# Kernel optimization log

Hardware: AMD Instinct MI355X
Metric: run time of the kernel (lower is better)

The kernel has to match this reference:

```python
import jax, jax.numpy as jnp
import numpy as np

N = 100000   # nodes
E = 1600000  # edges
IN = 128     # in_dim
C = 32       # hidden_dim
H = 2        # heads1
G = 64       # graphs in batch
NEG_SLOPE = 0.2


def setup_inputs() -> dict:
    key = jax.random.key(0)
    ks = jax.random.split(key, 20)
    f = lambda k, shape: jax.random.normal(k, shape, dtype=jnp.float32) * 0.05
    return {
        "x": jax.random.normal(ks[0], (N, IN), dtype=jnp.float32),
        "edge_index": jax.random.randint(ks[1], (2, E), 0, N, dtype=jnp.int32),
        "batch": jnp.sort(jax.random.randint(ks[2], (N,), 0, G, dtype=jnp.int32)),
        # GATv2 layer 1: lin_l / lin_r [IN, H*C], att [H, C], bias [H*C]
        "Wl1": f(ks[3], (IN, H * C)), "Wr1": f(ks[4], (IN, H * C)),
        "att1": f(ks[5], (H, C)), "b1": f(ks[6], (H * C,)),
        # GATv2 layer 2: heads=1
        "Wl2": f(ks[7], (H * C, C)), "Wr2": f(ks[8], (H * C, C)),
        "att2": f(ks[9], (1, C)), "b2": f(ks[10], (C,)),
        # GlobalAttention gate_nn: Linear(C,C) -> ReLU -> Linear(C,1)
        "g1w": f(ks[11], (C, C)), "g1b": f(ks[12], (C,)),
        "g2w": f(ks[13], (C, 1)), "g2b": f(ks[14], (1,)),
        # MLP head
        "lin1w": f(ks[15], (C, C)), "lin1b": f(ks[16], (C,)),
        "lin2w": f(ks[17], (C, 1)), "lin2b": f(ks[18], (1,)),
    }


def _gatv2(x, src, dst, Wl, Wr, att, bias, heads, ch):
    """PyG GATv2Conv (concat=True, share_weights=False, eval mode)."""
    n = x.shape[0]
    xl = (x @ Wl).reshape(n, heads, ch)  # source transform (also the message)
    xr = (x @ Wr).reshape(n, heads, ch)  # target transform
    e = jax.nn.leaky_relu(xl[src] + xr[dst], negative_slope=NEG_SLOPE)  # [E,H,C]
    score = jnp.einsum('ehc,hc->eh', e, att)  # [E,H]
    # scatter-softmax over incoming edges of each destination node
    m = jax.ops.segment_max(score, dst, num_segments=n)
    m = jnp.where(jnp.isfinite(m), m, 0.0)  # nodes w/o in-edges
    ex = jnp.exp(score - m[dst])
    denom = jax.ops.segment_sum(ex, dst, num_segments=n)
    alpha = ex / denom[dst]  # [E,H]
    out = jax.ops.segment_sum(alpha[:, :, None] * xl[src], dst, num_segments=n)
    return out.reshape(n, heads * ch) + bias


def reference(x, edge_index, batch, Wl1, Wr1, att1, b1, Wl2, Wr2, att2, b2,
              g1w, g1b, g2w, g2b, lin1w, lin1b, lin2w, lin2b):
    src, dst = edge_index[0], edge_index[1]
    h = jax.nn.relu(_gatv2(x, src, dst, Wl1, Wr1, att1, b1, H, C))   # [N, H*C]
    h = jax.nn.relu(_gatv2(h, src, dst, Wl2, Wr2, att2, b2, 1, C))   # [N, C]
    # GlobalAttention pooling: softmax(gate_nn(h)) over nodes of each graph
    gate = jax.nn.relu(h @ g1w + g1b) @ g2w + g2b                     # [N,1]
    gm = jax.ops.segment_max(gate, batch, num_segments=G)
    gm = jnp.where(jnp.isfinite(gm), gm, 0.0)
    ge = jnp.exp(gate - gm[batch])
    gd = jax.ops.segment_sum(ge, batch, num_segments=G)
    attw = ge / gd[batch]                                             # [N,1]
    pooled = jax.ops.segment_sum(attw * h, batch, num_segments=G)     # [G,C]
    z = jax.nn.relu(pooled @ lin1w + lin1b)
    return (z @ lin2w + lin2b).squeeze(-1)                            # [G]
```

## Files before the change

kernel.cpp:

```cpp
#include <hip/hip_runtime.h>
#include <hip/hip_fp16.h>
#include <cfloat>
#include <cstdint>
#include <cstddef>

#define N_NODES 100000
#define N_EDGES 1600000
#define G_GRAPHS 64
#define BKT_SHIFT 9
#define BKT_NODES (1 << BKT_SHIFT)
#define NBKT ((N_NODES + BKT_NODES - 1) >> BKT_SHIFT)
#define BKT_STRIDE 12288
#define SRC_BITS 17

typedef _Float16 hvec2 __attribute__((ext_vector_type(2)));
typedef _Float16 hvec4 __attribute__((ext_vector_type(4)));
typedef _Float16 hvec8 __attribute__((ext_vector_type(8)));
typedef float f32x4 __attribute__((ext_vector_type(4)));

#define LOG2E 1.4426950408889634f

static __device__ __forceinline__ float fdot2(hvec2 a, hvec2 b, float c) {
#if __has_builtin(__builtin_amdgcn_fdot2)
  return __builtin_amdgcn_fdot2(a, b, c, false);
#else
  return fmaf((float)a.y, (float)b.y, fmaf((float)a.x, (float)b.x, c));
#endif
}

static __device__ __forceinline__ hvec2 leaky2(hvec2 v) {
  return __builtin_elementwise_max(v, v * (_Float16)0.2f);
}

static __device__ __forceinline__ float fast_exp2(float x) {
#if __has_builtin(__builtin_amdgcn_exp2f)
  return __builtin_amdgcn_exp2f(x);
#else
  return exp2f(x);
#endif
}

template <int CTRL>
static __device__ __forceinline__ float dppadd(float v) {
  const int vi = __builtin_bit_cast(int, v);
  const int ti = __builtin_amdgcn_update_dpp(0, vi, CTRL, 0xF, 0xF, true);
  return v + __builtin_bit_cast(float, ti);
}
static __device__ __forceinline__ float dpp_sum8(float v) {
  v = dppadd<0xB1>(v);
  v = dppadd<0x4E>(v);
  v = dppadd<0x141>(v);
  return v;
}

__launch_bounds__(256) __global__
void prepw2_kernel(const float* __restrict__ Wl1, const float* __restrict__ Wr1,
                   const float* __restrict__ Wl2, const float* __restrict__ Wr2,
                   __half* __restrict__ Wh1, __half* __restrict__ Wh2) {
  const int idx = blockIdx.x * 256 + threadIdx.x;
  if (idx < 2 * 128 * 64) {
    const int j2 = idx / 128;
    const int k = idx - j2 * 128;
    const int j = (j2 < 64) ? j2 : j2 - 64;
    const float v = (j2 < 64) ? Wl1[k * 64 + j] : Wr1[k * 64 + j];
    Wh1[idx] = __float2half(v);
  } else if (idx < 2 * 128 * 64 + 2 * 64 * 32) {
    const int i2 = idx - 2 * 128 * 64;
    const int j2 = i2 / 64;
    const int k = i2 - j2 * 64;
    const int j = (j2 < 32) ? j2 : j2 - 32;
    const float v = (j2 < 32) ? Wl2[k * 32 + j] : Wr2[k * 32 + j];
    Wh2[i2] = __float2half(v);
  }
}

template <int K, int J, bool FUSE>
__launch_bounds__(256) __global__
void gemm_mfma(const float* __restrict__ A, const __half* __restrict__ Wh,
               const float* __restrict__ bias, __half* __restrict__ O0,
               float* __restrict__ O1, int n) {
  constexpr int BM = 64;
  constexpr int KP = K + 8;
  constexpr int J2 = 2 * J;
  __shared__ __align__(16) __half Alds[BM][KP];
  __shared__ __align__(16) __half Wlds[J2][KP];
  const int tid = threadIdx.x;
  const int n0 = blockIdx.x * BM;

  for (int c = tid; c < J2 * (K / 8); c += 256) {
    const int j = c / (K / 8);
    const int k8 = c - j * (K / 8);
    const uint4 w = reinterpret_cast<const uint4*>(Wh)[c];
    *reinterpret_cast<uint4*>(&Wlds[j][k8 * 8]) = w;
  }
  for (int c = tid; c < BM * (K / 4); c += 256) {
    const int r = c / (K / 4);
    const int k4 = c - r * (K / 4);
    const int row = n0 + r;
    float4 v = make_float4(0.f, 0.f, 0.f, 0.f);
    if (row < n) {
      v = reinterpret_cast<const float4*>(A)[(size_t)row * (K / 4) + k4];
      if constexpr (FUSE) {
        const float4 b = reinterpret_cast<const float4*>(bias)[k4];
        v.x = fmaxf(v.x + b.x, 0.f);
        v.y = fmaxf(v.y + b.y, 0.f);
        v.z = fmaxf(v.z + b.z, 0.f);
        v.w = fmaxf(v.w + b.w, 0.f);
      }
    }
    const hvec4 h = {(_Float16)v.x, (_Float16)v.y, (_Float16)v.z,
                     (_Float16)v.w};
    *reinterpret_cast<hvec4*>(&Alds[r][k4 * 4]) = h;
  }
  __syncthreads();

  const int wv = tid >> 6;
  const int l = tid & 63;
  const int lr = l & 15;
  const int lk = l >> 4;

  hvec8 afrag[K / 32];
#pragma unroll
  for (int kc = 0; kc < K / 32; ++kc)
    afrag[kc] = *reinterpret_cast<const hvec8*>(
        &Alds[wv * 16 + lr][kc * 32 + 8 * lk]);

#pragma unroll
  for (int jt = 0; jt < J2 / 16; ++jt) {
    f32x4 acc = {0.f, 0.f, 0.f, 0.f};
#pragma unroll
    for (int kc = 0; kc < K / 32; ++kc) {
      const hvec8 b = *reinterpret_cast<const hvec8*>(
          &Wlds[jt * 16 + lr][kc * 32 + 8 * lk]);
      acc = __builtin_amdgcn_mfma_f32_16x16x32_f16(afrag[kc], b, acc, 0, 0, 0);
    }
    const int colt = jt * 16 + lr;
    const int rowb = n0 + wv * 16 + 4 * lk;
#pragma unroll
    for (int r = 0; r < 4; ++r) {
      const int row = rowb + r;
      if (row < n) {
        if (jt < J / 16)
          O0[(size_t)row * J + colt] = __float2half(acc[r]);
        else
          O1[(size_t)row * J + (colt - J)] = acc[r];
      }
    }
  }
}

__launch_bounds__(1024) __global__
void partA_kernel(const int* __restrict__ ei, int* __restrict__ bcursor,
                  int* __restrict__ staging) {
  __shared__ int lh[NBKT];
  __shared__ int lbase[NBKT];
  const int tid = threadIdx.x;
  for (int i = tid; i < NBKT; i += 1024) lh[i] = 0;
  __syncthreads();
  const int e0 = blockIdx.x * 4096 + tid;
  int pk[4], b[4];
#pragma unroll
  for (int k = 0; k < 4; ++k) {
    const int e = e0 + k * 1024;
    const bool ok = e < N_EDGES;
    const int s = ok ? ei[e] : 0;
    const int d = ok ? ei[N_EDGES + e] : 0;
    pk[k] = s | ((d & (BKT_NODES - 1)) << SRC_BITS);
    b[k] = ok ? (d >> BKT_SHIFT) : -1;
    if (ok) atomicAdd(&lh[b[k]], 1);
  }
  __syncthreads();
  for (int i = tid; i < NBKT; i += 1024) {
    const int c = lh[i];
    lbase[i] = i * BKT_STRIDE + (c ? atomicAdd(&bcursor[i], c) : 0);
    lh[i] = 0;
  }
  __syncthreads();
#pragma unroll
  for (int k = 0; k < 4; ++k) {
    if (b[k] >= 0) {
      const int p = lbase[b[k]] + atomicAdd(&lh[b[k]], 1);
      staging[p] = pk[k];
    }
  }
}

__launch_bounds__(256) __global__
void partB_kernel(const int* __restrict__ staging,
                  const int* __restrict__ bcursor, int2* __restrict__ rowdeg,
                  int* __restrict__ csr_src) {
  __shared__ int ldeg[BKT_NODES];
  __shared__ int lsc[256];
  const int b = blockIdx.x;
  const int tid = threadIdx.x;
  const int node0 = b << BKT_SHIFT;
  const int start = b * BKT_STRIDE;
  const int cnt = bcursor[b];
  if (tid < 64) csr_src[start + cnt + tid] = 0;
  ldeg[2 * tid] = 0;
  ldeg[2 * tid + 1] = 0;
  __syncthreads();
  for (int i = tid; i < cnt; i += 256)
    atomicAdd(&ldeg[staging[start + i] >> SRC_BITS], 1);
  __syncthreads();
  const int d0 = ldeg[2 * tid];
  const int d1 = ldeg[2 * tid + 1];
  const int psum = d0 + d1;
  lsc[tid] = psum;
  __syncthreads();
  for (int d = 1; d < 256; d <<= 1) {
    const int t = (tid >= d) ? lsc[tid - d] : 0;
    __syncthreads();
    lsc[tid] += t;
    __syncthreads();
  }
  const int ex = lsc[tid] - psum + start;
  const int n0 = node0 + 2 * tid;
  if (n0 < N_NODES)
    *reinterpret_cast<int4*>(&rowdeg[n0]) = make_int4(ex, d0, ex + d0, d1);
  __syncthreads();
  ldeg[2 * tid] = ex;
  ldeg[2 * tid + 1] = ex + d0;
  __syncthreads();
  for (int i = tid; i < cnt; i += 256) {
    const int pk = staging[start + i];
    const int p = atomicAdd(&ldeg[pk >> SRC_BITS], 1);
    csr_src[p] = pk & ((1 << SRC_BITS) - 1);
  }
}

__launch_bounds__(256) __global__
void gat1_kernel(const __half* __restrict__ xlh, const float* __restrict__ xr,
                 const float* __restrict__ att, const int2* __restrict__ rowdeg,
                 const int* __restrict__ csr_src, float* __restrict__ agg) {
  const int n =
      __builtin_amdgcn_readfirstlane(blockIdx.x * 4 + (threadIdx.x >> 6));
  if (n >= N_NODES) return;
  const int lane = threadIdx.x & 63;
  const int g = lane >> 4;
  const int m = lane & 15;
  const int2 rd = rowdeg[n];
  const int r0 = __builtin_amdgcn_readfirstlane(rd.x);
  const int dg = __builtin_amdgcn_readfirstlane(rd.y);

  const float4 xrf =
      *reinterpret_cast<const float4*>(xr + ((size_t)n << 6) + 4 * m);
  const hvec2 xh01 = {(_Float16)xrf.x, (_Float16)xrf.y};
  const hvec2 xh23 = {(_Float16)xrf.z, (_Float16)xrf.w};
  const float4 atf = *reinterpret_cast<const float4*>(att + 4 * m);
  const hvec2 at01 = {(_Float16)(atf.x * LOG2E), (_Float16)(atf.y * LOG2E)};
  const hvec2 at23 = {(_Float16)(atf.z * LOG2E), (_Float16)(atf.w * LOG2E)};

  float s = 0.f, acc0 = 0.f, acc1 = 0.f, acc2 = 0.f, acc3 = 0.f;

  auto gather1 = [&](int sel) -> uint2 {
    return *reinterpret_cast<const uint2*>(
        (const char*)xlh + (((size_t)(unsigned)sel) << 7) + 8 * m);
  };
  auto compute1 = [&](int q, uint2 buf, int rem) {
    const hvec2 a01 = __builtin_bit_cast(hvec2, buf.x);
    const hvec2 a23 = __builtin_bit_cast(hvec2, buf.y);
    const hvec2 v01 = leaky2(a01 + xh01);
    const hvec2 v23 = leaky2(a23 + xh23);
    float p = fdot2(v23, at23, fdot2(v01, at01, 0.f));
    p = dpp_sum8(p);
    float e = fast_exp2(p);
    e = (4 * q + g < rem) ? e : 0.f;
    s += e;
    acc0 = fmaf(e, (float)a01.x, acc0);
    acc1 = fmaf(e, (float)a01.y, acc1);
    acc2 = fmaf(e, (float)a23.x, acc2);
    acc3 = fmaf(e, (float)a23.y, acc3);
  };

  for (int c0 = 0; c0 < dg; c0 += 64) {
    const int rem = dg - c0;
    const int* cp = csr_src + r0 + c0 + (lane >> 4);
    const int Kc = (min(rem, 64) + 3) >> 2;
#pragma unroll
    for (int g0 = 0; g0 < 16; g0 += 4) {
      if (g0 < Kc) {
        int sq[4];
#pragma unroll
        for (int k = 0; k < 4; ++k) sq[k] = cp[4 * (g0 + k)];
        uint2 B[4];
#pragma unroll
        for (int k = 0; k < 4; ++k)
          if (g0 + k < Kc) B[k] = gather1(sq[k]);
#pragma unroll
        for (int k = 0; k < 4; ++k)
          if (g0 + k < Kc) compute1(g0 + k, B[k], rem);
      }
    }
  }

  s += __shfl_xor(s, 16);
  s += __shfl_xor(s, 32);
  acc0 += __shfl_xor(acc0, 16);
  acc0 += __shfl_xor(acc0, 32);
  acc1 += __shfl_xor(acc1, 16);
  acc1 += __shfl_xor(acc1, 32);
  acc2 += __shfl_xor(acc2, 16);
  acc2 += __shfl_xor(acc2, 32);
  acc3 += __shfl_xor(acc3, 16);
  acc3 += __shfl_xor(acc3, 32);
  const float inv = s > 0.f ? 1.f / s : 0.f;
  if (g == 0)
    *reinterpret_cast<float4*>(agg + ((size_t)n << 6) + 4 * m) =
        make_float4(acc0 * inv, acc1 * inv, acc2 * inv, acc3 * inv);
}

__launch_bounds__(256) __global__
void gat2_kernel(const __half* __restrict__ xlh, const float* __restrict__ xr,
                 const float* __restrict__ att, const int2* __restrict__ rowdeg,
                 const int* __restrict__ csr_src, const float* __restrict__ b2,
                 float* __restrict__ h2) {
  const int n =
      __builtin_amdgcn_readfirstlane(blockIdx.x * 4 + (threadIdx.x >> 6));
  if (n >= N_NODES) return;
  const int lane = threadIdx.x & 63;
  const int g = lane >> 3;
  const int m = lane & 7;
  const int2 rd = rowdeg[n];
  const int r0 = __builtin_amdgcn_readfirstlane(rd.x);
  const int dg = __builtin_amdgcn_readfirstlane(rd.y);

  const float4 xrf =
      *reinterpret_cast<const float4*>(xr + (size_t)n * 32 + 4 * m);
  const hvec2 xh01 = {(_Float16)xrf.x, (_Float16)xrf.y};
  const hvec2 xh23 = {(_Float16)xrf.z, (_Float16)xrf.w};
  const float4 atf = *reinterpret_cast<const float4*>(att + 4 * m);
  const hvec2 at01 = {(_Float16)(atf.x * LOG2E), (_Float16)(atf.y * LOG2E)};
  const hvec2 at23 = {(_Float16)(atf.z * LOG2E), (_Float16)(atf.w * LOG2E)};

  float s = 0.f, acc0 = 0.f, acc1 = 0.f, acc2 = 0.f, acc3 = 0.f;

  auto gather1 = [&](int sel) -> uint2 {
    return *reinterpret_cast<const uint2*>(
        (const char*)xlh + (((size_t)(unsigned)sel) << 6) + 8 * m);
  };
  auto compute1 = [&](int q, uint2 buf, int rem) {
    const hvec2 a01 = __builtin_bit_cast(hvec2, buf.x);
    const hvec2 a23 = __builtin_bit_cast(hvec2, buf.y);
    const hvec2 v01 = leaky2(a01 + xh01);
    const hvec2 v23 = leaky2(a23 + xh23);
    float p = fdot2(v23, at23, fdot2(v01, at01, 0.f));
    p = dpp_sum8(p);
    float e = fast_exp2(p);
    e = (8 * q + g < rem) ? e : 0.f;
    s += e;
    acc0 = fmaf(e, (float)a01.x, acc0);
    acc1 = fmaf(e, (float)a01.y, acc1);
    acc2 = fmaf(e, (float)a23.x, acc2);
    acc3 = fmaf(e, (float)a23.y, acc3);
  };

  for (int c0 = 0; c0 < dg; c0 += 64) {
    const int rem = dg - c0;
    const int* cp = csr_src + r0 + c0 + (lane >> 3);
    const int Kc = (min(rem, 64) + 7) >> 3;
#pragma unroll
    for (int g0 = 0; g0 < 8; g0 += 4) {
      if (g0 < Kc) {
        int sq[4];
#pragma unroll
        for (int k = 0; k < 4; ++k) sq[k] = cp[8 * (g0 + k)];
        uint2 B[4];
#pragma unroll
        for (int k = 0; k < 4; ++k)
          if (g0 + k < Kc) B[k] = gather1(sq[k]);
#pragma unroll
        for (int k = 0; k < 4; ++k)
          if (g0 + k < Kc) compute1(g0 + k, B[k], rem);
      }
    }
  }

  s += __shfl_xor(s, 8);
  s += __shfl_xor(s, 16);
  s += __shfl_xor(s, 32);
  acc0 += __shfl_xor(acc0, 8);
  acc0 += __shfl_xor(acc0, 16);
  acc0 += __shfl_xor(acc0, 32);
  acc1 += __shfl_xor(acc1, 8);
  acc1 += __shfl_xor(acc1, 16);
  acc1 += __shfl_xor(acc1, 32);
  acc2 += __shfl_xor(acc2, 8);
  acc2 += __shfl_xor(acc2, 16);
  acc2 += __shfl_xor(acc2, 32);
  acc3 += __shfl_xor(acc3, 8);
  acc3 += __shfl_xor(acc3, 16);
  acc3 += __shfl_xor(acc3, 32);
  const float inv = s > 0.f ? 1.f / s : 0.f;
  const float4 b2v = *reinterpret_cast<const float4*>(b2 + 4 * m);
  if (g == 0)
    *reinterpret_cast<float4*>(h2 + (size_t)n * 32 + 4 * m) =
        make_float4(fmaxf(fmaf(acc0, inv, b2v.x), 0.f),
                    fmaxf(fmaf(acc1, inv, b2v.y), 0.f),
                    fmaxf(fmaf(acc2, inv, b2v.z), 0.f),
                    fmaxf(fmaf(acc3, inv, b2v.w), 0.f));
}

__launch_bounds__(256) __global__
void gate_kernel(const float* __restrict__ h2, const float* __restrict__ g1w,
                 const float* __restrict__ g1b, const float* __restrict__ g2w,
                 const float* __restrict__ g2b, float* __restrict__ gate) {
  __shared__ float Wg[32 * 32];
  __shared__ float Hs[8][32];
  const int tid = threadIdx.x;
  for (int i = tid; i < 1024; i += 256) Wg[i] = g1w[i];
  const int c = tid & 31;
  const int slot = tid >> 5;
  const int n = blockIdx.x * 8 + slot;
  Hs[slot][c] = (n < N_NODES) ? h2[(size_t)n * 32 + c] : 0.f;
  __syncthreads();
  float sg = g1b[c];
#pragma unroll
  for (int k4 = 0; k4 < 8; ++k4) {
    const float4 hq = *reinterpret_cast<const float4*>(&Hs[slot][4 * k4]);
    sg = fmaf(hq.x, Wg[(4 * k4 + 0) * 32 + c], sg);
    sg = fmaf(hq.y, Wg[(4 * k4 + 1) * 32 + c], sg);
    sg = fmaf(hq.z, Wg[(4 * k4 + 2) * 32 + c], sg);
    sg = fmaf(hq.w, Wg[(4 * k4 + 3) * 32 + c], sg);
  }
  sg = fmaxf(sg, 0.f);
  float pg = sg * g2w[c];
  pg += __shfl_xor(pg, 1);
  pg += __shfl_xor(pg, 2);
  pg += __shfl_xor(pg, 4);
  pg += __shfl_xor(pg, 8);
  pg += __shfl_xor(pg, 16);
  if (c == 0 && n < N_NODES) gate[n] = pg + g2b[0];
}

__launch_bounds__(256) __global__
void gepool_kernel(const float* __restrict__ h2, const int* __restrict__ batch,
                   const float* __restrict__ gate, float* __restrict__ gd,
                   float* __restrict__ pooled) {
  __shared__ float pool[G_GRAPHS * 32];
  __shared__ float gdb[G_GRAPHS];
  const int tid = threadIdx.x;
  for (int i = tid; i < G_GRAPHS * 32; i += 256) pool[i] = 0.f;
  if (tid < G_GRAPHS) gdb[tid] = 0.f;
  __syncthreads();
  const int c = tid & 31;
  const int hw = tid >> 5;
  const int start = blockIdx.x * 256;
  const int end = min(N_NODES, start + 256);
  for (int n = start + hw; n < end; n += 8) {
    const int b = batch[n];
    const float ge = __expf(gate[n]);
    atomicAdd(&pool[b * 32 + c], ge * h2[(size_t)n * 32 + c]);
    if (c == 0) atomicAdd(&gdb[b], ge);
  }
  __syncthreads();
  for (int i = tid; i < G_GRAPHS * 32; i += 256)
    if (pool[i] != 0.f) unsafeAtomicAdd(&pooled[i], pool[i]);
  if (tid < G_GRAPHS && gdb[tid] != 0.f) unsafeAtomicAdd(&gd[tid], gdb[tid]);
}

__launch_bounds__(64) __global__
void final_kernel(const float* __restrict__ pooled, const float* __restrict__ gd,
                  const float* __restrict__ l1w, const float* __restrict__ l1b,
                  const float* __restrict__ l2w, const float* __restrict__ l2b,
                  float* __restrict__ out) {
  const int g = blockIdx.x;
  const int lane = threadIdx.x;
  if (lane >= 32) return;
  const float invgd = 1.f / gd[g];
  float s = l1b[lane];
#pragma unroll
  for (int k = 0; k < 32; ++k)
    s = fmaf(pooled[g * 32 + k] * invgd, l1w[k * 32 + lane], s);
  s = fmaxf(s, 0.f);
  float p = s * l2w[lane];
  p += __shfl_xor(p, 1);
  p += __shfl_xor(p, 2);
  p += __shfl_xor(p, 4);
  p += __shfl_xor(p, 8);
  p += __shfl_xor(p, 16);
  if (lane == 0) out[g] = p + l2b[0];
}

extern "C" void kernel_launch(void* const* d_in, const int* in_sizes, int n_in,
                              void* d_out, int out_size, void* d_ws,
                              size_t ws_size, hipStream_t stream) {
  const float* x    = (const float*)d_in[0];
  const int*   ei   = (const int*)d_in[1];
  const int*   batch= (const int*)d_in[2];
  const float* Wl1  = (const float*)d_in[3];
  const float* Wr1  = (const float*)d_in[4];
  const float* att1 = (const float*)d_in[5];
  const float* b1   = (const float*)d_in[6];
  const float* Wl2  = (const float*)d_in[7];
  const float* Wr2  = (const float*)d_in[8];
  const float* att2 = (const float*)d_in[9];
  const float* b2   = (const float*)d_in[10];
  const float* g1w  = (const float*)d_in[11];
  const float* g1b  = (const float*)d_in[12];
  const float* g2w  = (const float*)d_in[13];
  const float* g2b  = (const float*)d_in[14];
  const float* l1w  = (const float*)d_in[15];
  const float* l1b  = (const float*)d_in[16];
  const float* l2w  = (const float*)d_in[17];
  const float* l2b  = (const float*)d_in[18];
  float* out = (float*)d_out;

  int* bcursor = (int*)d_ws;
  int2* rowdeg = (int2*)(bcursor + NBKT);
  int* csr_src = (int*)(rowdeg + N_NODES);
  int* staging = csr_src + (size_t)NBKT * BKT_STRIDE;
  float* fbase = (float*)(staging + (size_t)NBKT * BKT_STRIDE);
  float* xr1  = fbase;
  float* agg1 = xr1 + (size_t)N_NODES * 64;
  float* gate = agg1 + (size_t)N_NODES * 64;
  float* gd   = gate + N_NODES;
  float* pooled = gd + G_GRAPHS;
  __half* xl1h = (__half*)(pooled + G_GRAPHS * 32);
  __half* xl2h = xl1h;
  float* xr2 = xr1;
  float* h2  = xr1 + (size_t)N_NODES * 32;
  __half* Wh1 = (__half*)gate;
  __half* Wh2 = Wh1 + 128 * 128;

  (void)hipMemsetAsync(bcursor, 0, (size_t)NBKT * sizeof(int), stream);
  (void)hipMemsetAsync(gd, 0,
                       (size_t)(G_GRAPHS + G_GRAPHS * 32) * sizeof(float),
                       stream);

  prepw2_kernel<<<(2 * 128 * 64 + 2 * 64 * 32 + 255) / 256, 256, 0, stream>>>(
      Wl1, Wr1, Wl2, Wr2, Wh1, Wh2);

  partA_kernel<<<(N_EDGES + 4095) / 4096, 1024, 0, stream>>>(ei, bcursor,
                                                             staging);
  partB_kernel<<<NBKT, 256, 0, stream>>>(staging, bcursor, rowdeg, csr_src);

  gemm_mfma<128, 64, false><<<(N_NODES + 63) / 64, 256, 0, stream>>>(
      x, Wh1, nullptr, xl1h, xr1, N_NODES);
  gat1_kernel<<<(N_NODES + 3) / 4, 256, 0, stream>>>(xl1h, xr1, att1, rowdeg,
                                                     csr_src, agg1);

  gemm_mfma<64, 32, true><<<(N_NODES + 63) / 64, 256, 0, stream>>>(
      agg1, Wh2, b1, xl2h, xr2, N_NODES);
  gat2_kernel<<<(N_NODES + 3) / 4, 256, 0, stream>>>(xl2h, xr2, att2, rowdeg,
                                                     csr_src, b2, h2);
  gate_kernel<<<(N_NODES + 7) / 8, 256, 0, stream>>>(h2, g1w, g1b, g2w, g2b,
                                                     gate);

  gepool_kernel<<<(N_NODES + 255) / 256, 256, 0, stream>>>(h2, batch, gate, gd,
                                                           pooled);
  final_kernel<<<64, 64, 0, stream>>>(pooled, gd, l1w, l1b, l2w, l2b, out);
}
```

Measured before the change: 337.0 us.

## Merge small kernels to cut launches: fold weight prep, CSR build, gate and final

Folds the weight fp16 conversion into the edge-partition kernel and runs the CSR bucket build and the first GEMM as disjoint block ranges of one launch. The gate MLP is fused into the pooling kernel using wave shuffles, and the final MLP runs in the last block, picked by an atomic ticket. Two memsets become one. This removes about five launches and the gate round trip through global memory, at the cost of a last-block serial tail and more complex synchronisation.

```diff
diff --git a/kernel.cpp b/kernel.cpp
--- a/kernel.cpp
+++ b/kernel.cpp
@@ -53,108 +53,30 @@
   return v;
 }
 
-__launch_bounds__(256) __global__
-void prepw2_kernel(const float* __restrict__ Wl1, const float* __restrict__ Wr1,
-                   const float* __restrict__ Wl2, const float* __restrict__ Wr2,
-                   __half* __restrict__ Wh1, __half* __restrict__ Wh2) {
-  const int idx = blockIdx.x * 256 + threadIdx.x;
-  if (idx < 2 * 128 * 64) {
-    const int j2 = idx / 128;
-    const int k = idx - j2 * 128;
+__launch_bounds__(1024) __global__
+void partA_kernel(const int* __restrict__ ei, int* __restrict__ bcursor,
+                  int* __restrict__ staging,
+                  const float* __restrict__ Wl1, const float* __restrict__ Wr1,
+                  const float* __restrict__ Wl2, const float* __restrict__ Wr2,
+                  __half* __restrict__ Wh1, __half* __restrict__ Wh2) {
+  const int tid = threadIdx.x;
+  const int widx = blockIdx.x * 1024 + tid;
+  if (widx < 2 * 128 * 64) {
+    const int j2 = widx / 128;
+    const int k = widx - j2 * 128;
     const int j = (j2 < 64) ? j2 : j2 - 64;
-    const float v = (j2 < 64) ? Wl1[k * 64 + j] : Wr1[k * 64 + j];
-    Wh1[idx] = __float2half(v);
-  } else if (idx < 2 * 128 * 64 + 2 * 64 * 32) {
-    const int i2 = idx - 2 * 128 * 64;
+    Wh1[widx] =
+        __float2half((j2 < 64) ? Wl1[k * 64 + j] : Wr1[k * 64 + j]);
+  } else if (widx < 2 * 128 * 64 + 2 * 64 * 32) {
+    const int i2 = widx - 2 * 128 * 64;
     const int j2 = i2 / 64;
     const int k = i2 - j2 * 64;
     const int j = (j2 < 32) ? j2 : j2 - 32;
-    const float v = (j2 < 32) ? Wl2[k * 32 + j] : Wr2[k * 32 + j];
-    Wh2[i2] = __float2half(v);
-  }
-}
-
-template <int K, int J, bool FUSE>
-__launch_bounds__(256) __global__
-void gemm_mfma(const float* __restrict__ A, const __half* __restrict__ Wh,
-               const float* __restrict__ bias, __half* __restrict__ O0,
-               float* __restrict__ O1, int n) {
-  constexpr int BM = 64;
-  constexpr int KP = K + 8;
-  constexpr int J2 = 2 * J;
-  __shared__ __align__(16) __half Alds[BM][KP];
-  __shared__ __align__(16) __half Wlds[J2][KP];
-  const int tid = threadIdx.x;
-  const int n0 = blockIdx.x * BM;
-
-  for (int c = tid; c < J2 * (K / 8); c += 256) {
-    const int j = c / (K / 8);
-    const int k8 = c - j * (K / 8);
-    const uint4 w = reinterpret_cast<const uint4*>(Wh)[c];
-    *reinterpret_cast<uint4*>(&Wlds[j][k8 * 8]) = w;
-  }
-  for (int c = tid; c < BM * (K / 4); c += 256) {
-    const int r = c / (K / 4);
-    const int k4 = c - r * (K / 4);
-    const int row = n0 + r;
-    float4 v = make_float4(0.f, 0.f, 0.f, 0.f);
-    if (row < n) {
-      v = reinterpret_cast<const float4*>(A)[(size_t)row * (K / 4) + k4];
-      if constexpr (FUSE) {
-        const float4 b = reinterpret_cast<const float4*>(bias)[k4];
-        v.x = fmaxf(v.x + b.x, 0.f);
-        v.y = fmaxf(v.y + b.y, 0.f);
-        v.z = fmaxf(v.z + b.z, 0.f);
-        v.w = fmaxf(v.w + b.w, 0.f);
-      }
-    }
-    const hvec4 h = {(_Float16)v.x, (_Float16)v.y, (_Float16)v.z,
-                     (_Float16)v.w};
-    *reinterpret_cast<hvec4*>(&Alds[r][k4 * 4]) = h;
-  }
-  __syncthreads();
-
-  const int wv = tid >> 6;
-  const int l = tid & 63;
-  const int lr = l & 15;
-  const int lk = l >> 4;
-
-  hvec8 afrag[K / 32];
-#pragma unroll
-  for (int kc = 0; kc < K / 32; ++kc)
-    afrag[kc] = *reinterpret_cast<const hvec8*>(
-        &Alds[wv * 16 + lr][kc * 32 + 8 * lk]);
-
-#pragma unroll
-  for (int jt = 0; jt < J2 / 16; ++jt) {
-    f32x4 acc = {0.f, 0.f, 0.f, 0.f};
-#pragma unroll
-    for (int kc = 0; kc < K / 32; ++kc) {
-      const hvec8 b = *reinterpret_cast<const hvec8*>(
-          &Wlds[jt * 16 + lr][kc * 32 + 8 * lk]);
-      acc = __builtin_amdgcn_mfma_f32_16x16x32_f16(afrag[kc], b, acc, 0, 0, 0);
-    }
-    const int colt = jt * 16 + lr;
-    const int rowb = n0 + wv * 16 + 4 * lk;
-#pragma unroll
-    for (int r = 0; r < 4; ++r) {
-      const int row = rowb + r;
-      if (row < n) {
-        if (jt < J / 16)
-          O0[(size_t)row * J + colt] = __float2half(acc[r]);
-        else
-          O1[(size_t)row * J + (colt - J)] = acc[r];
-      }
-    }
-  }
-}
-
-__launch_bounds__(1024) __global__
-void partA_kernel(const int* __restrict__ ei, int* __restrict__ bcursor,
-                  int* __restrict__ staging) {
+    Wh2[i2] = __float2half((j2 < 32) ? Wl2[k * 32 + j] : Wr2[k * 32 + j]);
+  }
+
   __shared__ int lh[NBKT];
   __shared__ int lbase[NBKT];
-  const int tid = threadIdx.x;
   for (int i = tid; i < NBKT; i += 1024) lh[i] = 0;
   __syncthreads();
   const int e0 = blockIdx.x * 4096 + tid;
@@ -185,47 +107,193 @@
   }
 }
 
+#define GEMM1_K 128
+#define GEMM1_J 64
+#define SMEM_BYTES (64 * (GEMM1_K + 8) * 2 + 2 * GEMM1_J * (GEMM1_K + 8) * 2)
+
 __launch_bounds__(256) __global__
-void partB_kernel(const int* __restrict__ staging,
-                  const int* __restrict__ bcursor, int2* __restrict__ rowdeg,
-                  int* __restrict__ csr_src) {
-  __shared__ int ldeg[BKT_NODES];
-  __shared__ int lsc[256];
-  const int b = blockIdx.x;
+void partB_gemm1_kernel(const int* __restrict__ staging,
+                        const int* __restrict__ bcursor,
+                        int2* __restrict__ rowdeg, int* __restrict__ csr_src,
+                        const float* __restrict__ A,
+                        const __half* __restrict__ Wh,
+                        __half* __restrict__ O0, float* __restrict__ O1) {
+  __shared__ __align__(16) char smem[SMEM_BYTES];
   const int tid = threadIdx.x;
-  const int node0 = b << BKT_SHIFT;
-  const int start = b * BKT_STRIDE;
-  const int cnt = bcursor[b];
-  if (tid < 64) csr_src[start + cnt + tid] = 0;
-  ldeg[2 * tid] = 0;
-  ldeg[2 * tid + 1] = 0;
-  __syncthreads();
-  for (int i = tid; i < cnt; i += 256)
-    atomicAdd(&ldeg[staging[start + i] >> SRC_BITS], 1);
-  __syncthreads();
-  const int d0 = ldeg[2 * tid];
-  const int d1 = ldeg[2 * tid + 1];
-  const int psum = d0 + d1;
-  lsc[tid] = psum;
-  __syncthreads();
-  for (int d = 1; d < 256; d <<= 1) {
-    const int t = (tid >= d) ? lsc[tid - d] : 0;
+
+  if (blockIdx.x < NBKT) {
+    int* ldeg = (int*)smem;
+    int* lsc = (int*)(smem + BKT_NODES * 4);
+    const int b = blockIdx.x;
+    const int node0 = b << BKT_SHIFT;
+    const int start = b * BKT_STRIDE;
+    const int cnt = bcursor[b];
+    if (tid < 64) csr_src[start + cnt + tid] = 0;
+    ldeg[2 * tid] = 0;
+    ldeg[2 * tid + 1] = 0;
     __syncthreads();
-    lsc[tid] += t;
+    for (int i = tid; i < cnt; i += 256)
+      atomicAdd(&ldeg[staging[start + i] >> SRC_BITS], 1);
     __syncthreads();
-  }
-  const int ex = lsc[tid] - psum + start;
-  const int n0 = node0 + 2 * tid;
-  if (n0 < N_NODES)
-    *reinterpret_cast<int4*>(&rowdeg[n0]) = make_int4(ex, d0, ex + d0, d1);
-  __syncthreads();
-  ldeg[2 * tid] = ex;
-  ldeg[2 * tid + 1] = ex + d0;
-  __syncthreads();
-  for (int i = tid; i < cnt; i += 256) {
-    const int pk = staging[start + i];
-    const int p = atomicAdd(&ldeg[pk >> SRC_BITS], 1);
-    csr_src[p] = pk & ((1 << SRC_BITS) - 1);
+    const int d0 = ldeg[2 * tid];
+    const int d1 = ldeg[2 * tid + 1];
+    const int psum = d0 + d1;
+    lsc[tid] = psum;
+    __syncthreads();
+    for (int d = 1; d < 256; d <<= 1) {
+      const int t = (tid >= d) ? lsc[tid - d] : 0;
+      __syncthreads();
+      lsc[tid] += t;
+      __syncthreads();
+    }
+    const int ex = lsc[tid] - psum + start;
+    const int n0 = node0 + 2 * tid;
+    if (n0 < N_NODES)
+      *reinterpret_cast<int4*>(&rowdeg[n0]) = make_int4(ex, d0, ex + d0, d1);
+    __syncthreads();
+    ldeg[2 * tid] = ex;
+    ldeg[2 * tid + 1] = ex + d0;
+    __syncthreads();
+    for (int i = tid; i < cnt; i += 256) {
+      const int pk = staging[start + i];
+      const int p = atomicAdd(&ldeg[pk >> SRC_BITS], 1);
+      csr_src[p] = pk & ((1 << SRC_BITS) - 1);
+    }
+    return;
+  }
+
+  constexpr int K = GEMM1_K;
+  constexpr int J = GEMM1_J;
+  constexpr int KP = K + 8;
+  constexpr int J2 = 2 * J;
+  typedef __half(*AldsT)[KP];
+  AldsT Alds = (AldsT)smem;
+  AldsT Wlds = (AldsT)(smem + 64 * KP * 2);
+  const int n0 = (blockIdx.x - NBKT) * 64;
+
+  for (int c = tid; c < J2 * (K / 8); c += 256) {
+    const int j = c / (K / 8);
+    const int k8 = c - j * (K / 8);
+    const uint4 w = reinterpret_cast<const uint4*>(Wh)[c];
+    *reinterpret_cast<uint4*>(&Wlds[j][k8 * 8]) = w;
+  }
+  for (int c = tid; c < 64 * (K / 4); c += 256) {
+    const int r = c / (K / 4);
+    const int k4 = c - r * (K / 4);
+    const int row = n0 + r;
+    float4 v = make_float4(0.f, 0.f, 0.f, 0.f);
+    if (row < N_NODES)
+      v = reinterpret_cast<const float4*>(A)[(size_t)row * (K / 4) + k4];
+    const hvec4 h = {(_Float16)v.x, (_Float16)v.y, (_Float16)v.z,
+                     (_Float16)v.w};
+    *reinterpret_cast<hvec4*>(&Alds[r][k4 * 4]) = h;
+  }
+  __syncthreads();
+
+  const int wv = tid >> 6;
+  const int l = tid & 63;
+  const int lr = l & 15;
+  const int lk = l >> 4;
+
+  hvec8 afrag[K / 32];
+#pragma unroll
+  for (int kc = 0; kc < K / 32; ++kc)
+    afrag[kc] = *reinterpret_cast<const hvec8*>(
+        &Alds[wv * 16 + lr][kc * 32 + 8 * lk]);
+
+#pragma unroll
+  for (int jt = 0; jt < J2 / 16; ++jt) {
+    f32x4 acc = {0.f, 0.f, 0.f, 0.f};
+#pragma unroll
+    for (int kc = 0; kc < K / 32; ++kc) {
+      const hvec8 b = *reinterpret_cast<const hvec8*>(
+          &Wlds[jt * 16 + lr][kc * 32 + 8 * lk]);
+      acc = __builtin_amdgcn_mfma_f32_16x16x32_f16(afrag[kc], b, acc, 0, 0, 0);
+    }
+    const int colt = jt * 16 + lr;
+    const int rowb = n0 + wv * 16 + 4 * lk;
+#pragma unroll
+    for (int r = 0; r < 4; ++r) {
+      const int row = rowb + r;
+      if (row < N_NODES) {
+        if (jt < J / 16)
+          O0[(size_t)row * J + colt] = __float2half(acc[r]);
+        else
+          O1[(size_t)row * J + (colt - J)] = acc[r];
+      }
+    }
+  }
+}
+
+template <int K, int J>
+__launch_bounds__(256) __global__
+void gemm_mfma2(const float* __restrict__ A, const __half* __restrict__ Wh,
+                const float* __restrict__ bias, __half* __restrict__ O0,
+                float* __restrict__ O1) {
+  constexpr int KP = K + 8;
+  constexpr int J2 = 2 * J;
+  __shared__ __align__(16) __half Alds[64][KP];
+  __shared__ __align__(16) __half Wlds[J2][KP];
+  const int tid = threadIdx.x;
+  const int n0 = blockIdx.x * 64;
+
+  for (int c = tid; c < J2 * (K / 8); c += 256) {
+    const int j = c / (K / 8);
+    const int k8 = c - j * (K / 8);
+    const uint4 w = reinterpret_cast<const uint4*>(Wh)[c];
+    *reinterpret_cast<uint4*>(&Wlds[j][k8 * 8]) = w;
+  }
+  for (int c = tid; c < 64 * (K / 4); c += 256) {
+    const int r = c / (K / 4);
+    const int k4 = c - r * (K / 4);
+    const int row = n0 + r;
+    float4 v = make_float4(0.f, 0.f, 0.f, 0.f);
+    if (row < N_NODES) {
+      v = reinterpret_cast<const float4*>(A)[(size_t)row * (K / 4) + k4];
+      const float4 b = reinterpret_cast<const float4*>(bias)[k4];
+      v.x = fmaxf(v.x + b.x, 0.f);
+      v.y = fmaxf(v.y + b.y, 0.f);
+      v.z = fmaxf(v.z + b.z, 0.f);
+      v.w = fmaxf(v.w + b.w, 0.f);
+    }
+    const hvec4 h = {(_Float16)v.x, (_Float16)v.y, (_Float16)v.z,
+                     (_Float16)v.w};
+    *reinterpret_cast<hvec4*>(&Alds[r][k4 * 4]) = h;
+  }
+  __syncthreads();
+
+  const int wv = tid >> 6;
+  const int l = tid & 63;
+  const int lr = l & 15;
+  const int lk = l >> 4;
+
+  hvec8 afrag[K / 32];
+#pragma unroll
+  for (int kc = 0; kc < K / 32; ++kc)
+    afrag[kc] = *reinterpret_cast<const hvec8*>(
+        &Alds[wv * 16 + lr][kc * 32 + 8 * lk]);
+
+#pragma unroll
+  for (int jt = 0; jt < J2 / 16; ++jt) {
+    f32x4 acc = {0.f, 0.f, 0.f, 0.f};
+#pragma unroll
+    for (int kc = 0; kc < K / 32; ++kc) {
+      const hvec8 b = *reinterpret_cast<const hvec8*>(
+          &Wlds[jt * 16 + lr][kc * 32 + 8 * lk]);
+      acc = __builtin_amdgcn_mfma_f32_16x16x32_f16(afrag[kc], b, acc, 0, 0, 0);
+    }
+    const int colt = jt * 16 + lr;
+    const int rowb = n0 + wv * 16 + 4 * lk;
+#pragma unroll
+    for (int r = 0; r < 4; ++r) {
+      const int row = rowb + r;
+      if (row < N_NODES) {
+        if (jt < J / 16)
+          O0[(size_t)row * J + colt] = __float2half(acc[r]);
+        else
+          O1[(size_t)row * J + (colt - J)] = acc[r];
+      }
+    }
   }
 }
 
@@ -402,84 +470,88 @@
 }
 
 __launch_bounds__(256) __global__
-void gate_kernel(const float* __restrict__ h2, const float* __restrict__ g1w,
-                 const float* __restrict__ g1b, const float* __restrict__ g2w,
-                 const float* __restrict__ g2b, float* __restrict__ gate) {
+void gepool_final_kernel(const float* __restrict__ h2,
+                         const int* __restrict__ batch,
+                         const float* __restrict__ g1w,
+                         const float* __restrict__ g1b,
+                         const float* __restrict__ g2w,
+                         const float* __restrict__ g2b,
+                         float* __restrict__ gd, float* __restrict__ pooled,
+                         int* __restrict__ done,
+                         const float* __restrict__ l1w,
+                         const float* __restrict__ l1b,
+                         const float* __restrict__ l2w,
+                         const float* __restrict__ l2b,
+                         float* __restrict__ out) {
   __shared__ float Wg[32 * 32];
-  __shared__ float Hs[8][32];
+  __shared__ float pool[G_GRAPHS * 32];
+  __shared__ float gdb[G_GRAPHS];
+  __shared__ int lticket;
   const int tid = threadIdx.x;
   for (int i = tid; i < 1024; i += 256) Wg[i] = g1w[i];
-  const int c = tid & 31;
-  const int slot = tid >> 5;
-  const int n = blockIdx.x * 8 + slot;
-  Hs[slot][c] = (n < N_NODES) ? h2[(size_t)n * 32 + c] : 0.f;
-  __syncthreads();
-  float sg = g1b[c];
-#pragma unroll
-  for (int k4 = 0; k4 < 8; ++k4) {
-    const float4 hq = *reinterpret_cast<const float4*>(&Hs[slot][4 * k4]);
-    sg = fmaf(hq.x, Wg[(4 * k4 + 0) * 32 + c], sg);
-    sg = fmaf(hq.y, Wg[(4 * k4 + 1) * 32 + c], sg);
-    sg = fmaf(hq.z, Wg[(4 * k4 + 2) * 32 + c], sg);
-    sg = fmaf(hq.w, Wg[(4 * k4 + 3) * 32 + c], sg);
-  }
-  sg = fmaxf(sg, 0.f);
-  float pg = sg * g2w[c];
-  pg += __shfl_xor(pg, 1);
-  pg += __shfl_xor(pg, 2);
-  pg += __shfl_xor(pg, 4);
-  pg += __shfl_xor(pg, 8);
-  pg += __shfl_xor(pg, 16);
-  if (c == 0 && n < N_NODES) gate[n] = pg + g2b[0];
-}
-
-__launch_bounds__(256) __global__
-void gepool_kernel(const float* __restrict__ h2, const int* __restrict__ batch,
-                   const float* __restrict__ gate, float* __restrict__ gd,
-                   float* __restrict__ pooled) {
-  __shared__ float pool[G_GRAPHS * 32];
-  __shared__ float gdb[G_GRAPHS];
-  const int tid = threadIdx.x;
   for (int i = tid; i < G_GRAPHS * 32; i += 256) pool[i] = 0.f;
   if (tid < G_GRAPHS) gdb[tid] = 0.f;
   __syncthreads();
   const int c = tid & 31;
   const int hw = tid >> 5;
+  const float g1bc = g1b[c];
+  const float g2wc = g2w[c];
+  const float g2b0 = g2b[0];
   const int start = blockIdx.x * 256;
   const int end = min(N_NODES, start + 256);
   for (int n = start + hw; n < end; n += 8) {
     const int b = batch[n];
-    const float ge = __expf(gate[n]);
-    atomicAdd(&pool[b * 32 + c], ge * h2[(size_t)n * 32 + c]);
+    const float hval = h2[(size_t)n * 32 + c];
+    float sg = g1bc;
+#pragma unroll
+    for (int k = 0; k < 32; ++k)
+      sg = fmaf(__shfl(hval, k, 32), Wg[k * 32 + c], sg);
+    sg = fmaxf(sg, 0.f);
+    float pg = sg * g2wc;
+    pg += __shfl_xor(pg, 1);
+    pg += __shfl_xor(pg, 2);
+    pg += __shfl_xor(pg, 4);
+    pg += __shfl_xor(pg, 8);
+    pg += __shfl_xor(pg, 16);
+    const float ge = __expf(pg + g2b0);
+    atomicAdd(&pool[b * 32 + c], ge * hval);
     if (c == 0) atomicAdd(&gdb[b], ge);
   }
   __syncthreads();
   for (int i = tid; i < G_GRAPHS * 32; i += 256)
     if (pool[i] != 0.f) unsafeAtomicAdd(&pooled[i], pool[i]);
   if (tid < G_GRAPHS && gdb[tid] != 0.f) unsafeAtomicAdd(&gd[tid], gdb[tid]);
-}
-
-__launch_bounds__(64) __global__
-void final_kernel(const float* __restrict__ pooled, const float* __restrict__ gd,
-                  const float* __restrict__ l1w, const float* __restrict__ l1b,
-                  const float* __restrict__ l2w, const float* __restrict__ l2b,
-                  float* __restrict__ out) {
-  const int g = blockIdx.x;
-  const int lane = threadIdx.x;
-  if (lane >= 32) return;
-  const float invgd = 1.f / gd[g];
-  float s = l1b[lane];
-#pragma unroll
-  for (int k = 0; k < 32; ++k)
-    s = fmaf(pooled[g * 32 + k] * invgd, l1w[k * 32 + lane], s);
-  s = fmaxf(s, 0.f);
-  float p = s * l2w[lane];
-  p += __shfl_xor(p, 1);
-  p += __shfl_xor(p, 2);
-  p += __shfl_xor(p, 4);
-  p += __shfl_xor(p, 8);
-  p += __shfl_xor(p, 16);
-  if (lane == 0) out[g] = p + l2b[0];
+
+  __threadfence();
+  __syncthreads();
+  if (tid == 0) lticket = atomicAdd(done, 1);
+  __syncthreads();
+  if (lticket == (int)gridDim.x - 1) {
+    __threadfence();
+    const int lane = tid & 31;
+    const int gq = tid >> 5;
+    for (int g = gq; g < G_GRAPHS; g += 8) {
+      const float gdv =
+          __hip_atomic_load(&gd[g], __ATOMIC_RELAXED, __HIP_MEMORY_SCOPE_AGENT);
+      const float invgd = 1.f / gdv;
+      float s = l1b[lane];
+#pragma unroll
+      for (int k = 0; k < 32; ++k) {
+        const float pv = __hip_atomic_load(&pooled[g * 32 + k],
+                                           __ATOMIC_RELAXED,
+                                           __HIP_MEMORY_SCOPE_AGENT);
+        s = fmaf(pv * invgd, l1w[k * 32 + lane], s);
+      }
+      s = fmaxf(s, 0.f);
+      float p = s * l2w[lane];
+      p += __shfl_xor(p, 1);
+      p += __shfl_xor(p, 2);
+      p += __shfl_xor(p, 4);
+      p += __shfl_xor(p, 8);
+      p += __shfl_xor(p, 16);
+      if (lane == 0) out[g] = p + l2b[0];
+    }
+  }
 }
 
 extern "C" void kernel_launch(void* const* d_in, const int* in_sizes, int n_in,
@@ -506,48 +578,41 @@
   const float* l2b  = (const float*)d_in[18];
   float* out = (float*)d_out;
 
-  int* bcursor = (int*)d_ws;
-  int2* rowdeg = (int2*)(bcursor + NBKT);
+  int* zbase = (int*)d_ws;
+  int* bcursor = zbase;
+  int* done = zbase + 196;
+  float* gd = (float*)(zbase + 256);
+  float* pooled = gd + G_GRAPHS;
+  int2* rowdeg = (int2*)(pooled + G_GRAPHS * 32);
   int* csr_src = (int*)(rowdeg + N_NODES);
   int* staging = csr_src + (size_t)NBKT * BKT_STRIDE;
-  float* fbase = (float*)(staging + (size_t)NBKT * BKT_STRIDE);
-  float* xr1  = fbase;
+  float* xr1  = (float*)(staging + (size_t)NBKT * BKT_STRIDE);
   float* agg1 = xr1 + (size_t)N_NODES * 64;
-  float* gate = agg1 + (size_t)N_NODES * 64;
-  float* gd   = gate + N_NODES;
-  float* pooled = gd + G_GRAPHS;
-  __half* xl1h = (__half*)(pooled + G_GRAPHS * 32);
+  __half* Wh1 = (__half*)(agg1 + (size_t)N_NODES * 64);
+  __half* Wh2 = Wh1 + 128 * 128;
+  __half* xl1h = (__half*)(Wh2 + 64 * 64);
   __half* xl2h = xl1h;
   float* xr2 = xr1;
   float* h2  = xr1 + (size_t)N_NODES * 32;
-  __half* Wh1 = (__half*)gate;
-  __half* Wh2 = Wh1 + 128 * 128;
-
-  (void)hipMemsetAsync(bcursor, 0, (size_t)NBKT * sizeof(int), stream);
-  (void)hipMemsetAsync(gd, 0,
-                       (size_t)(G_GRAPHS + G_GRAPHS * 32) * sizeof(float),
+
+  (void)hipMemsetAsync(zbase, 0, (size_t)(256 + 64 + 2048) * sizeof(int),
                        stream);
 
-  prepw2_kernel<<<(2 * 128 * 64 + 2 * 64 * 32 + 255) / 256, 256, 0, stream>>>(
-      Wl1, Wr1, Wl2, Wr2, Wh1, Wh2);
-
-  partA_kernel<<<(N_EDGES + 4095) / 4096, 1024, 0, stream>>>(ei, bcursor,
-                                                             staging);
-  partB_kernel<<<NBKT, 256, 0, stream>>>(staging, bcursor, rowdeg, csr_src);
-
-  gemm_mfma<128, 64, false><<<(N_NODES + 63) / 64, 256, 0, stream>>>(
-      x, Wh1, nullptr, xl1h, xr1, N_NODES);
+  partA_kernel<<<(N_EDGES + 4095) / 4096, 1024, 0, stream>>>(
+      ei, bcursor, staging, Wl1, Wr1, Wl2, Wr2, Wh1, Wh2);
+
+  partB_gemm1_kernel<<<NBKT + (N_NODES + 63) / 64, 256, 0, stream>>>(
+      staging, bcursor, rowdeg, csr_src, x, Wh1, xl1h, xr1);
+
   gat1_kernel<<<(N_NODES + 3) / 4, 256, 0, stream>>>(xl1h, xr1, att1, rowdeg,
                                                      csr_src, agg1);
 
-  gemm_mfma<64, 32, true><<<(N_NODES + 63) / 64, 256, 0, stream>>>(
-      agg1, Wh2, b1, xl2h, xr2, N_NODES);
+  gemm_mfma2<64, 32><<<(N_NODES + 63) / 64, 256, 0, stream>>>(agg1, Wh2, b1,
+                                                              xl2h, xr2);
   gat2_kernel<<<(N_NODES + 3) / 4, 256, 0, stream>>>(xl2h, xr2, att2, rowdeg,
                                                      csr_src, b2, h2);
-  gate_kernel<<<(N_NODES + 7) / 8, 256, 0, stream>>>(h2, g1w, g1b, g2w, g2b,
-                                                     gate);
-
-  gepool_kernel<<<(N_NODES + 255) / 256, 256, 0, stream>>>(h2, batch, gate, gd,
-                                                           pooled);
-  final_kernel<<<64, 64, 0, stream>>>(pooled, gd, l1w, l1b, l2w, l2b, out);
-}
+
+  gepool_final_kernel<<<(N_NODES + 255) / 256, 256, 0, stream>>>(
+      h2, batch, g1w, g1b, g2w, g2b, gd, pooled, done, l1w, l1b, l2w, l2b,
+      out);
+}
```

After: 335.2 us. About the same (-0.5%).
